# Kernel optimization log

Hardware: AMD Instinct MI355X
Metric: run time of the kernel (lower is better)

The kernel has to match this reference:

```python
import jax, jax.numpy as jnp
import numpy as np

B, S, E, H = 4, 2048, 1024, 16
D = E // H  # head_dim = 64

def setup_inputs() -> dict:
    key = jax.random.key(0)
    k1, k2, k3, k4, k5 = jax.random.split(key, 5)
    x = jax.random.normal(k1, (B, S, E), dtype=jnp.float32)
    # causal mask, broadcast over batch and heads; mask==0 -> -inf
    mask = jnp.tril(jnp.ones((S, S), dtype=jnp.int32))[None, None, :, :]
    Wqkv = jax.random.normal(k2, (E, 3 * E), dtype=jnp.float32) * (1.0 / np.sqrt(E))
    bqkv = jax.random.normal(k3, (3 * E,), dtype=jnp.float32) * 0.02
    Wo = jax.random.normal(k4, (E, E), dtype=jnp.float32) * (1.0 / np.sqrt(E))
    bo = jax.random.normal(k5, (E,), dtype=jnp.float32) * 0.02
    return {"x": x, "mask": mask, "Wqkv": Wqkv, "bqkv": bqkv, "Wo": Wo, "bo": bo}

def reference(x, mask, Wqkv, bqkv, Wo, bo):
    b, s, e = x.shape
    scale = 1.0 / np.sqrt(D)
    qkv = x @ Wqkv + bqkv                      # [b,s,3e]
    qkv = qkv.reshape(b, s, H, 3 * D).transpose(0, 2, 1, 3)  # [b,h,s,3d]
    q, k, v = jnp.split(qkv, 3, axis=-1)       # each [b,h,s,d]
    scores = jnp.einsum('bnqd,bnkd->bnqk', q, k) * scale
    scores = jnp.where(mask == 0, -jnp.inf, scores)
    probs = jax.nn.softmax(scores, axis=-1)
    attn = jnp.einsum('bnqk,bnkd->bnqd', probs, v)  # [b,h,s,d]
    # Faithful to source: reshape (b,h,s,d) -> (b,s,e) WITHOUT transposing back
    attn = attn.reshape(b, s, e)
    return attn @ Wo + bo
```

## Files before the change

### kernel.cpp

```cpp
#include <hip/hip_runtime.h>

typedef __attribute__((ext_vector_type(8))) short bf16x8;
typedef __attribute__((ext_vector_type(4))) float f32x4;
typedef __attribute__((ext_vector_type(2))) unsigned int u32x2;
typedef __attribute__((ext_vector_type(4))) unsigned int u32x4;

#define MFMA16(a, b, c) __builtin_amdgcn_mfma_f32_16x16x32_bf16((a), (b), (c), 0, 0, 0)

#define S_LEN 2048
#define NHEAD 16
#define DHEAD 64
#define BH    64
#define MROWS 8192

__device__ __forceinline__ unsigned short f2bf(float f) {
  unsigned int u = __builtin_bit_cast(unsigned int, f);
  u += 0x7FFFu + ((u >> 16) & 1u);
  return (unsigned short)(u >> 16);
}

__device__ __forceinline__ void gl_lds16(const void* g, void* l) {
  __builtin_amdgcn_global_load_lds(
      (const __attribute__((address_space(1))) void*)g,
      (__attribute__((address_space(3))) void*)l, 16, 0, 0);
}

__device__ __forceinline__ unsigned int pkbf(float lo, float hi) {
  unsigned int ulo = __builtin_bit_cast(unsigned int, lo) + 0x8000u;
  unsigned int uhi = __builtin_bit_cast(unsigned int, hi) + 0x8000u;
  return __builtin_amdgcn_perm(uhi, ulo, 0x07060302u);
}

__global__ __launch_bounds__(256) void cast_bf16(const float* __restrict__ src,
                                                 unsigned short* __restrict__ dst, int n) {
  int i = (blockIdx.x * 256 + threadIdx.x) * 4;
  if (i + 3 < n) {
    f32x4 v = *(const f32x4*)(src + i);
    unsigned long long pk =
        (unsigned long long)f2bf(v[0]) |
        ((unsigned long long)f2bf(v[1]) << 16) |
        ((unsigned long long)f2bf(v[2]) << 32) |
        ((unsigned long long)f2bf(v[3]) << 48);
    *(unsigned long long*)(dst + i) = pk;
  }
}

__global__ __launch_bounds__(256) void transpose_cast(const float* __restrict__ src,
                                                      unsigned short* __restrict__ dst,
                                                      int R, int C) {
  __shared__ float tile[32][33];
  int c0 = blockIdx.x * 32, r0 = blockIdx.y * 32;
  int tx = threadIdx.x, ty = threadIdx.y;
  for (int i = 0; i < 32; i += 8)
    tile[ty + i][tx] = src[(size_t)(r0 + ty + i) * C + c0 + tx];
  __syncthreads();
  for (int i = 0; i < 32; i += 8)
    dst[(size_t)(c0 + ty + i) * R + r0 + tx] = f2bf(tile[tx][ty + i]);
}

__global__ __launch_bounds__(256) void transpose_cast_qkv(const float* __restrict__ src,
                                                          unsigned short* __restrict__ dst) {
  __shared__ float tile[32][33];
  int c0 = blockIdx.x * 32, r0 = blockIdx.y * 32;
  int tx = threadIdx.x, ty = threadIdx.y;
  for (int i = 0; i < 32; i += 8)
    tile[ty + i][tx] = src[(size_t)(r0 + ty + i) * 3072 + c0 + tx];
  __syncthreads();
  for (int i = 0; i < 32; i += 8) {
    int oc = c0 + ty + i;
    int h = oc / 192, rr = oc % 192;
    int nc = ((rr >> 6) << 10) + (h << 6) + (rr & 63);
    dst[(size_t)nc * 1024 + r0 + tx] = f2bf(tile[tx][ty + i]);
  }
}

#define GEMM_CORE(A_, Bt_)                                                              \
  __shared__ unsigned short As[128 * 32];                                               \
  __shared__ unsigned short Bs[128 * 32];                                               \
  const int tid = threadIdx.x;                                                          \
  const int w = tid >> 6, lane = tid & 63, l15 = lane & 15, quad = lane >> 4;           \
  const int wm = w >> 1, wn = w & 1;                                                    \
  const int col0 = blockIdx.x * 128, row0 = blockIdx.y * 128;                           \
  f32x4 acc[4][4] = {};                                                                 \
  for (int kt = 0; kt < 32; ++kt) {                                                     \
    const int k0 = kt * 32;                                                             \
    for (int p = 0; p < 2; ++p) {                                                       \
      int c = p * 256 + tid;                                                            \
      int m = c >> 2, k8 = (c & 3) * 8;                                                 \
      void* ldsA = (char*)As + (size_t)(p * 256 + (tid & 192)) * 16;                    \
      void* ldsB = (char*)Bs + (size_t)(p * 256 + (tid & 192)) * 16;                    \
      gl_lds16(A_ + (size_t)(row0 + m) * 1024 + k0 + k8, ldsA);                         \
      gl_lds16(Bt_ + (size_t)(col0 + m) * 1024 + k0 + k8, ldsB);                        \
    }                                                                                   \
    __syncthreads();                                                                    \
    bf16x8 af[4], bfr[4];                                                               \
    for (int i = 0; i < 4; ++i)                                                         \
      af[i] = *(const bf16x8*)&As[(wm * 64 + i * 16 + l15) * 32 + quad * 8];            \
    for (int j = 0; j < 4; ++j)                                                         \
      bfr[j] = *(const bf16x8*)&Bs[(wn * 64 + j * 16 + l15) * 32 + quad * 8];           \
    for (int i = 0; i < 4; ++i)                                                         \
      for (int j = 0; j < 4; ++j)                                                       \
        acc[i][j] = MFMA16(af[i], bfr[j], acc[i][j]);                                   \
    __syncthreads();                                                                    \
  }


#define VM3 asm volatile("s_waitcnt vmcnt(3)" ::: "memory")
#define VM0 asm volatile("s_waitcnt vmcnt(0)" ::: "memory")
#define BAR __builtin_amdgcn_s_barrier()
#define SB  __builtin_amdgcn_sched_barrier(0)
#define SGB_G(m, n) __builtin_amdgcn_sched_group_barrier((m), (n), 0)

#define SGBPAT                                                                   \
  SGB_G(0x70, 3);                                                                \
  SGB_G(0x8, 2); SGB_G(0x100, 1); SGB_G(0x8, 2); SGB_G(0x100, 1);                \
  SGB_G(0x8, 2); SGB_G(0x100, 1); SGB_G(0x8, 2); SGB_G(0x100, 1);                \
  SGB_G(0x8, 2); SGB_G(0x100, 1); SGB_G(0x8, 2); SGB_G(0x100, 1);                \
  SGB_G(0x8, 2); SGB_G(0x100, 1); SGB_G(0x8, 2); SGB_G(0x100, 1)

#define STAGE3(T, KH, BUF)                                                       \
  do {                                                                           \
    const unsigned short* ga_ = a_src + (T) * 64 + (KH) * 32;                    \
    const unsigned short* gb_ = b_src + (T) * 64 + (KH) * 32;                    \
    char* la_ = SHB + (BUF) * 49152 + (KH) * 8192 + stgo;                        \
    char* lb_ = SHB + (BUF) * 49152 + 16384 + (KH) * 16384 + stgo;               \
    gl_lds16(ga_, la_);                                                          \
    gl_lds16(gb_, lb_);                                                          \
    gl_lds16(gb_ + 131072, lb_ + 8192);                                          \
  } while (0)

#define RDSET(S, BUF, KH)                                                        \
  do {                                                                           \
    const char* Ab_ = SHB + (BUF) * 49152 + (KH) * 8192 + abase;                 \
    const char* Bb_ = SHB + (BUF) * 49152 + 16384 + (KH) * 16384 + bbase;        \
    af##S##0 = *(const bf16x8*)(Ab_);                                            \
    af##S##1 = *(const bf16x8*)(Ab_ + 1024);                                     \
    af##S##2 = *(const bf16x8*)(Ab_ + 2048);                                     \
    af##S##3 = *(const bf16x8*)(Ab_ + 3072);                                     \
    bq##S##0 = *(const bf16x8*)(Bb_);                                            \
    bq##S##1 = *(const bf16x8*)(Bb_ + 1024);                                     \
    bq##S##2 = *(const bf16x8*)(Bb_ + 2048);                                     \
    bq##S##3 = *(const bf16x8*)(Bb_ + 3072);                                     \
  } while (0)

#define MFMA16S(S)                                                               \
  acc[0][0] = MFMA16(af##S##0, bq##S##0, acc[0][0]);                             \
  acc[0][1] = MFMA16(af##S##0, bq##S##1, acc[0][1]);                             \
  acc[0][2] = MFMA16(af##S##0, bq##S##2, acc[0][2]);                             \
  acc[0][3] = MFMA16(af##S##0, bq##S##3, acc[0][3]);                             \
  acc[1][0] = MFMA16(af##S##1, bq##S##0, acc[1][0]);                             \
  acc[1][1] = MFMA16(af##S##1, bq##S##1, acc[1][1]);                             \
  acc[1][2] = MFMA16(af##S##1, bq##S##2, acc[1][2]);                             \
  acc[1][3] = MFMA16(af##S##1, bq##S##3, acc[1][3]);                             \
  acc[2][0] = MFMA16(af##S##2, bq##S##0, acc[2][0]);                             \
  acc[2][1] = MFMA16(af##S##2, bq##S##1, acc[2][1]);                             \
  acc[2][2] = MFMA16(af##S##2, bq##S##2, acc[2][2]);                             \
  acc[2][3] = MFMA16(af##S##2, bq##S##3, acc[2][3]);                             \
  acc[3][0] = MFMA16(af##S##3, bq##S##0, acc[3][0]);                             \
  acc[3][1] = MFMA16(af##S##3, bq##S##1, acc[3][1]);                             \
  acc[3][2] = MFMA16(af##S##3, bq##S##2, acc[3][2]);                             \
  acc[3][3] = MFMA16(af##S##3, bq##S##3, acc[3][3])

#define WND(SP, STG_, VM_, RD_)                                                  \
  {                                                                              \
    STG_;                                                                        \
    __builtin_amdgcn_s_setprio(1);                                               \
    MFMA16S(SP);                                                                 \
    RD_;                                                                         \
    __builtin_amdgcn_s_setprio(0);                                               \
    SGBPAT;                                                                      \
    VM_; SB; BAR; SB;                                                            \
  }

__global__ __launch_bounds__(512, 2) void gemm_qkv(const unsigned short* __restrict__ A,
                                                   const unsigned short* __restrict__ Bt,
                                                   const float* __restrict__ bias,
                                                   unsigned short* __restrict__ Qb,
                                                   unsigned short* __restrict__ Kb,
                                                   unsigned short* __restrict__ Vtb) {
  __shared__ unsigned short SH[49152];
  char* SHB = (char*)SH;
  const int tid = threadIdx.x;
  const int w = tid >> 6, lane = tid & 63, l15 = lane & 15, quad = lane >> 4;
  const int wm = w >> 2, wn = w & 3;
  const int g = ((blockIdx.x & 7) * 96) + (blockIdx.x >> 3);
  const int bx = g % 12, by = g / 12;
  const int col0 = bx << 8, row0 = by << 7;

  const int qa = quad ^ ((l15 >> 1) & 3);
  const int abase = (wm * 64 + l15) * 64 + qa * 16;
  const int bbase = (wn * 64 + l15) * 64 + qa * 16;

  const int qsw = (tid & 3) ^ ((tid >> 3) & 3);
  const unsigned short* a_src = A + (size_t)(row0 + (tid >> 2)) * 1024 + qsw * 8;
  const unsigned short* b_src = Bt + (size_t)(col0 + (tid >> 2)) * 1024 + qsw * 8;
  const int stgo = (tid & ~63) * 16;

  f32x4 acc[4][4] = {};
  bf16x8 afA0, afA1, afA2, afA3, bqA0, bqA1, bqA2, bqA3;
  bf16x8 afB0, afB1, afB2, afB3, bqB0, bqB1, bqB2, bqB3;

  STAGE3(0, 0, 0); STAGE3(0, 1, 0); STAGE3(1, 0, 1);
  VM3; SB; BAR; SB;
  RDSET(A, 0, 0);

  #pragma unroll 1
  for (int jj = 0; jj < 7; ++jj) {
    const int J0 = 2 * jj;
    WND(A, STAGE3(J0 + 1, 1, 1), VM3, RDSET(B, 0, 1))
    WND(B, STAGE3(J0 + 2, 0, 0), VM3, RDSET(A, 1, 0))
    WND(A, STAGE3(J0 + 2, 1, 0), VM3, RDSET(B, 1, 1))
    WND(B, STAGE3(J0 + 3, 0, 1), VM3, RDSET(A, 0, 0))
  }
  WND(A, STAGE3(15, 1, 1), VM3, RDSET(B, 0, 1))
  WND(B, (void)0, VM0, RDSET(A, 1, 0))
  WND(A, (void)0, (void)0, RDSET(B, 1, 1))
  __builtin_amdgcn_s_setprio(1);
  MFMA16S(B);
  __builtin_amdgcn_s_setprio(0);
  __syncthreads();

  const int which = col0 >> 10;
  const int h = ((col0 + wn * 64) >> 6) & 15;
  const int b = row0 >> 11;
  const int srow0 = (row0 & 2047) + wm * 64;
  float bv[4];
  #pragma unroll
  for (int j = 0; j < 4; ++j) {
    int nc = col0 + wn * 64 + j * 16 + l15;
    int oc = ((nc >> 6) & 15) * 192 + (nc >> 10) * 64 + (nc & 63);
    bv[j] = bias[oc];
  }
  float* Ew = (float*)SHB + w * 1072;

  if (which < 2) {
    const float sc = (which == 0) ? 0.18033688011112042f : 1.0f;
    const int lr = lane >> 2, d0 = (lane & 3) * 16;
    unsigned short* base = (which == 0 ? Qb : Kb) + ((size_t)(b * 16 + h) * 2048 + srow0) * 64;
    #pragma unroll
    for (int i = 0; i < 4; ++i) {
      #pragma unroll
      for (int j = 0; j < 4; ++j)
        #pragma unroll
        for (int r = 0; r < 4; ++r)
          Ew[(quad * 4 + r) * 66 + j * 16 + l15] = (acc[i][j][r] + bv[j]) * sc;
      float v[16];
      #pragma unroll
      for (int c = 0; c < 4; ++c)
        *(f32x4*)&v[4 * c] = *(const f32x4*)&Ew[lr * 66 + d0 + 4 * c];
      u32x4 pk0 = {pkbf(v[0], v[1]), pkbf(v[2], v[3]), pkbf(v[4], v[5]), pkbf(v[6], v[7])};
      u32x4 pk1 = {pkbf(v[8], v[9]), pkbf(v[10], v[11]), pkbf(v[12], v[13]), pkbf(v[14], v[15])};
      unsigned short* dst = base + (size_t)(i * 16 + lr) * 64 + d0;
      *(u32x4*)dst = pk0;
      *(u32x4*)(dst + 8) = pk1;
    }
  } else {
    const int d = lane;
    unsigned short* base = Vtb + ((size_t)(b * 16 + h) * 64 + d) * 2048 + srow0;
    #pragma unroll
    for (int i = 0; i < 4; ++i) {
      #pragma unroll
      for (int j = 0; j < 4; ++j)
        #pragma unroll
        for (int r = 0; r < 4; ++r)
          Ew[(quad * 4 + r) * 66 + j * 16 + l15] = acc[i][j][r] + bv[j];
      float e[16];
      #pragma unroll
      for (int k = 0; k < 16; ++k) e[k] = Ew[k * 66 + d];
      u32x4 pk0 = {pkbf(e[0], e[1]), pkbf(e[2], e[3]), pkbf(e[4], e[5]), pkbf(e[6], e[7])};
      u32x4 pk1 = {pkbf(e[8], e[9]), pkbf(e[10], e[11]), pkbf(e[12], e[13]), pkbf(e[14], e[15])};
      unsigned short* dst = base + i * 16;
      *(u32x4*)dst = pk0;
      *(u32x4*)(dst + 8) = pk1;
    }
  }
}

__global__ __launch_bounds__(256) void gemm_out(const unsigned short* __restrict__ A,
                                                const unsigned short* __restrict__ Bt,
                                                const float* __restrict__ bias,
                                                float* __restrict__ out) {
  GEMM_CORE(A, Bt)
  for (int i = 0; i < 4; ++i) {
    int grow = row0 + wm * 64 + i * 16 + quad * 4;
    for (int j = 0; j < 4; ++j) {
      int gcol = col0 + wn * 64 + j * 16 + l15;
      float bvv = bias[gcol];
      for (int r = 0; r < 4; ++r)
        out[(size_t)(grow + r) * 1024 + gcol] = acc[i][j][r] + bvv;
    }
  }
}

__global__ __launch_bounds__(256) void attn_kernel(const unsigned short* __restrict__ Qb,
                                                   const unsigned short* __restrict__ Kb,
                                                   const unsigned short* __restrict__ Vtb,
                                                   unsigned short* __restrict__ attnout) {
  __shared__ unsigned short K0[64 * 32], K1[64 * 32];
  __shared__ unsigned short V0[64 * 32], V1[64 * 32];
  __shared__ unsigned short P0[4][4][512], P1[4][4][512];
  __shared__ float Lbc[4][64];

  const int tid = threadIdx.x;
  const int w = tid >> 6, lane = tid & 63, l15 = lane & 15, quad = lane >> 4;
  const int i2 = blockIdx.x >> 6;
  const int jj = ((i2 & 1) << 1) | ((i2 >> 1) & 1);
  const int qt = (i2 & 4) ? jj : 7 - jj;
  const int bh = blockIdx.x & 63;
  const int q0w = qt * 256 + w * 64;

  const unsigned short* Qg = Qb + (size_t)bh * S_LEN * DHEAD;
  const unsigned short* Kg = Kb + (size_t)bh * S_LEN * DHEAD;
  const unsigned short* Vg = Vtb + (size_t)bh * DHEAD * S_LEN;

  bf16x8 qf[4][2];
  #pragma unroll
  for (int sub = 0; sub < 4; ++sub) {
    const unsigned short* p = Qg + (size_t)(q0w + sub * 16 + l15) * DHEAD + quad * 8;
    qf[sub][0] = *(const bf16x8*)p;
    qf[sub][1] = *(const bf16x8*)(p + 32);
  }

  const int srow = tid >> 2, sc8 = (tid & 3) * 8;
  const unsigned short* kgb = Kg + srow * 64 + sc8;
  const unsigned short* vgb = Vg + (size_t)srow * S_LEN + sc8;
  const int wKo = srow * 32 + sc8;

  const int psw = (l15 & 3) ^ ((l15 >> 2) & 3);
  const int pw0 = l15 * 32 + (((quad >> 1) ^ psw) << 3) + ((quad & 1) << 2);
  const int pw1 = l15 * 32 + ((((quad >> 1) + 2) ^ psw) << 3) + ((quad & 1) << 2);
  const int pro = l15 * 32 + ((quad ^ psw) << 3);
  const int kvo = l15 * 32 + quad * 8;

  f32x4 oacc[4][4] = {};
  float lacc[4] = {0.f, 0.f, 0.f, 0.f};

  const int ktdiag = 4 * qt;
  const int nkt = ktdiag + 4;

  bf16x8 kr0 = *(const bf16x8*)kgb, kr1 = *(const bf16x8*)(kgb + 32);
  bf16x8 vr0 = *(const bf16x8*)vgb, vr1 = *(const bf16x8*)(vgb + 32);

  for (int kt = 0; kt < nkt; ++kt) {
    *(bf16x8*)&K0[wKo] = kr0;  *(bf16x8*)&K1[wKo] = kr1;
    *(bf16x8*)&V0[wKo] = vr0;  *(bf16x8*)&V1[wKo] = vr1;
    __syncthreads();
    if (kt + 1 < nkt) {
      const unsigned short* kp = kgb + (kt + 1) * 4096;
      const unsigned short* vp = vgb + (kt + 1) * 64;
      kr0 = *(const bf16x8*)kp;  kr1 = *(const bf16x8*)(kp + 32);
      vr0 = *(const bf16x8*)vp;  vr1 = *(const bf16x8*)(vp + 32);
    }

    const int t = kt - ktdiag;
    const bool act = (t < 0) || (w >= t);

    if (act) {
      if (t < 0) {
        #pragma unroll
        for (int jk = 0; jk < 4; ++jk) {
          bf16x8 kf0 = *(const bf16x8*)&K0[jk * 512 + kvo];
          bf16x8 kf1 = *(const bf16x8*)&K1[jk * 512 + kvo];
          #pragma unroll
          for (int sub = 0; sub < 4; ++sub) {
            f32x4 z = {};
            z = MFMA16(kf0, qf[sub][0], z);
            z = MFMA16(kf1, qf[sub][1], z);
            float e0 = __builtin_amdgcn_exp2f(z[0]);
            float e1 = __builtin_amdgcn_exp2f(z[1]);
            float e2 = __builtin_amdgcn_exp2f(z[2]);
            float e3 = __builtin_amdgcn_exp2f(z[3]);
            lacc[sub] += (e0 + e1) + (e2 + e3);
            unsigned short* pd = (jk < 2) ? P0[w][sub] : P1[w][sub];
            *(u32x2*)&pd[(jk & 1) ? pw1 : pw0] = (u32x2){pkbf(e0, e1), pkbf(e2, e3)};
          }
        }
      } else {
        const bool dg = (t == w);
        #pragma unroll
        for (int jk = 0; jk < 4; ++jk) {
          bf16x8 kf0 = *(const bf16x8*)&K0[jk * 512 + kvo];
          bf16x8 kf1 = *(const bf16x8*)&K1[jk * 512 + kvo];
          #pragma unroll
          for (int sub = 0; sub < 4; ++sub) {
            unsigned short* pd = (jk < 2) ? P0[w][sub] : P1[w][sub];
            unsigned int* dst = (unsigned int*)&pd[(jk & 1) ? pw1 : pw0];
            if (dg && jk > sub) { *(u32x2*)dst = (u32x2){0u, 0u}; continue; }
            f32x4 z = {};
            z = MFMA16(kf0, qf[sub][0], z);
            z = MFMA16(kf1, qf[sub][1], z);
            if (dg && jk == sub) {
              #pragma unroll
              for (int r = 0; r < 4; ++r)
                if (quad * 4 + r > l15) z[r] = -3e38f;
            }
            float e0 = __builtin_amdgcn_exp2f(z[0]);
            float e1 = __builtin_amdgcn_exp2f(z[1]);
            float e2 = __builtin_amdgcn_exp2f(z[2]);
            float e3 = __builtin_amdgcn_exp2f(z[3]);
            lacc[sub] += (e0 + e1) + (e2 + e3);
            *(u32x2*)dst = (u32x2){pkbf(e0, e1), pkbf(e2, e3)};
          }
        }
      }

      bf16x8 pf[4][2];
      #pragma unroll
      for (int sub = 0; sub < 4; ++sub) {
        pf[sub][0] = *(const bf16x8*)&P0[w][sub][pro];
        pf[sub][1] = *(const bf16x8*)&P1[w][sub][pro];
      }
      #pragma unroll
      for (int dt = 0; dt < 4; ++dt) {
        bf16x8 vb0 = *(const bf16x8*)&V0[dt * 512 + kvo];
        bf16x8 vb1 = *(const bf16x8*)&V1[dt * 512 + kvo];
        #pragma unroll
        for (int sub = 0; sub < 4; ++sub) {
          oacc[sub][dt] = MFMA16(pf[sub][0], vb0, oacc[sub][dt]);
          oacc[sub][dt] = MFMA16(pf[sub][1], vb1, oacc[sub][dt]);
        }
      }
    }
    __syncthreads();
  }

  #pragma unroll
  for (int sub = 0; sub < 4; ++sub) {
    float l = lacc[sub];
    l += __shfl_xor(l, 16);
    l += __shfl_xor(l, 32);
    if (quad == 0) Lbc[w][sub * 16 + l15] = l;
  }
  #pragma unroll
  for (int sub = 0; sub < 4; ++sub) {
    f32x4 l4 = *(const f32x4*)&Lbc[w][sub * 16 + quad * 4];
    int qbase = q0w + sub * 16 + quad * 4;
    unsigned short* dst = attnout + ((size_t)bh * S_LEN + qbase) * DHEAD;
    #pragma unroll
    for (int r = 0; r < 4; ++r) {
      float inv = __builtin_amdgcn_rcpf(l4[r]);
      #pragma unroll
      for (int dt = 0; dt < 4; ++dt)
        dst[(size_t)r * DHEAD + dt * 16 + l15] = f2bf(oacc[sub][dt][r] * inv);
    }
  }
}

extern "C" void kernel_launch(void* const* d_in, const int* in_sizes, int n_in,
                              void* d_out, int out_size, void* d_ws, size_t ws_size,
                              hipStream_t stream) {
  const float* x    = (const float*)d_in[0];
  const float* Wqkv = (const float*)d_in[2];
  const float* bqkv = (const float*)d_in[3];
  const float* Wo   = (const float*)d_in[4];
  const float* bo   = (const float*)d_in[5];
  float* out = (float*)d_out;

  char* ws = (char*)d_ws;
  unsigned short* Xbf   = (unsigned short*)(ws);
  unsigned short* WqkvT = (unsigned short*)(ws + 16777216);
  unsigned short* WoT   = (unsigned short*)(ws + 23068672);
  unsigned short* Qb    = (unsigned short*)(ws + 25165824);
  unsigned short* Kb    = (unsigned short*)(ws + 41943040);
  unsigned short* Vtb   = (unsigned short*)(ws + 58720256);
  unsigned short* Attn  = (unsigned short*)(ws + 75497472);

  cast_bf16<<<8192, 256, 0, stream>>>(x, Xbf, MROWS * 1024);
  transpose_cast_qkv<<<dim3(96, 32), dim3(32, 8), 0, stream>>>(Wqkv, WqkvT);
  transpose_cast<<<dim3(32, 32), dim3(32, 8), 0, stream>>>(Wo, WoT, 1024, 1024);
  gemm_qkv<<<768, 512, 0, stream>>>(Xbf, WqkvT, bqkv, Qb, Kb, Vtb);
  attn_kernel<<<512, 256, 0, stream>>>(Qb, Kb, Vtb, Attn);
  gemm_out<<<dim3(8, 64), 256, 0, stream>>>(Attn, WoT, bo, out);
}
```

Before: 275.2 us.

## Reuse pipelined 128x256 QKV GEMM main loop for output projection GEMM

```diff
diff --git a/kernel.cpp b/kernel.cpp
--- a/kernel.cpp
+++ b/kernel.cpp
@@ -73,36 +73,6 @@
     dst[(size_t)nc * 1024 + r0 + tx] = f2bf(tile[tx][ty + i]);
   }
 }
-
-#define GEMM_CORE(A_, Bt_)                                                              \
-  __shared__ unsigned short As[128 * 32];                                               \
-  __shared__ unsigned short Bs[128 * 32];                                               \
-  const int tid = threadIdx.x;                                                          \
-  const int w = tid >> 6, lane = tid & 63, l15 = lane & 15, quad = lane >> 4;           \
-  const int wm = w >> 1, wn = w & 1;                                                    \
-  const int col0 = blockIdx.x * 128, row0 = blockIdx.y * 128;                           \
-  f32x4 acc[4][4] = {};                                                                 \
-  for (int kt = 0; kt < 32; ++kt) {                                                     \
-    const int k0 = kt * 32;                                                             \
-    for (int p = 0; p < 2; ++p) {                                                       \
-      int c = p * 256 + tid;                                                            \
-      int m = c >> 2, k8 = (c & 3) * 8;                                                 \
-      void* ldsA = (char*)As + (size_t)(p * 256 + (tid & 192)) * 16;                    \
-      void* ldsB = (char*)Bs + (size_t)(p * 256 + (tid & 192)) * 16;                    \
-      gl_lds16(A_ + (size_t)(row0 + m) * 1024 + k0 + k8, ldsA);                         \
-      gl_lds16(Bt_ + (size_t)(col0 + m) * 1024 + k0 + k8, ldsB);                        \
-    }                                                                                   \
-    __syncthreads();                                                                    \
-    bf16x8 af[4], bfr[4];                                                               \
-    for (int i = 0; i < 4; ++i)                                                         \
-      af[i] = *(const bf16x8*)&As[(wm * 64 + i * 16 + l15) * 32 + quad * 8];            \
-    for (int j = 0; j < 4; ++j)                                                         \
-      bfr[j] = *(const bf16x8*)&Bs[(wn * 64 + j * 16 + l15) * 32 + quad * 8];           \
-    for (int i = 0; i < 4; ++i)                                                         \
-      for (int j = 0; j < 4; ++j)                                                       \
-        acc[i][j] = MFMA16(af[i], bfr[j], acc[i][j]);                                   \
-    __syncthreads();                                                                    \
-  }
 
 
 #define VM3 asm volatile("s_waitcnt vmcnt(3)" ::: "memory")
@@ -172,6 +142,26 @@
     VM_; SB; BAR; SB;                                                            \
   }
 
+#define GEMM256_KLOOP                                                            \
+  STAGE3(0, 0, 0); STAGE3(0, 1, 0); STAGE3(1, 0, 1);                             \
+  VM3; SB; BAR; SB;                                                              \
+  RDSET(A, 0, 0);                                                                \
+  _Pragma("unroll 1")                                                            \
+  for (int jj = 0; jj < 7; ++jj) {                                               \
+    const int J0 = 2 * jj;                                                       \
+    WND(A, STAGE3(J0 + 1, 1, 1), VM3, RDSET(B, 0, 1))                            \
+    WND(B, STAGE3(J0 + 2, 0, 0), VM3, RDSET(A, 1, 0))                            \
+    WND(A, STAGE3(J0 + 2, 1, 0), VM3, RDSET(B, 1, 1))                            \
+    WND(B, STAGE3(J0 + 3, 0, 1), VM3, RDSET(A, 0, 0))                            \
+  }                                                                              \
+  WND(A, STAGE3(15, 1, 1), VM3, RDSET(B, 0, 1))                                  \
+  WND(B, (void)0, VM0, RDSET(A, 1, 0))                                           \
+  WND(A, (void)0, (void)0, RDSET(B, 1, 1))                                       \
+  __builtin_amdgcn_s_setprio(1);                                                 \
+  MFMA16S(B);                                                                    \
+  __builtin_amdgcn_s_setprio(0);                                                 \
+  __syncthreads();
+
 __global__ __launch_bounds__(512, 2) void gemm_qkv(const unsigned short* __restrict__ A,
                                                    const unsigned short* __restrict__ Bt,
                                                    const float* __restrict__ bias,
@@ -200,25 +190,7 @@
   bf16x8 afA0, afA1, afA2, afA3, bqA0, bqA1, bqA2, bqA3;
   bf16x8 afB0, afB1, afB2, afB3, bqB0, bqB1, bqB2, bqB3;
 
-  STAGE3(0, 0, 0); STAGE3(0, 1, 0); STAGE3(1, 0, 1);
-  VM3; SB; BAR; SB;
-  RDSET(A, 0, 0);
-
-  #pragma unroll 1
-  for (int jj = 0; jj < 7; ++jj) {
-    const int J0 = 2 * jj;
-    WND(A, STAGE3(J0 + 1, 1, 1), VM3, RDSET(B, 0, 1))
-    WND(B, STAGE3(J0 + 2, 0, 0), VM3, RDSET(A, 1, 0))
-    WND(A, STAGE3(J0 + 2, 1, 0), VM3, RDSET(B, 1, 1))
-    WND(B, STAGE3(J0 + 3, 0, 1), VM3, RDSET(A, 0, 0))
-  }
-  WND(A, STAGE3(15, 1, 1), VM3, RDSET(B, 0, 1))
-  WND(B, (void)0, VM0, RDSET(A, 1, 0))
-  WND(A, (void)0, (void)0, RDSET(B, 1, 1))
-  __builtin_amdgcn_s_setprio(1);
-  MFMA16S(B);
-  __builtin_amdgcn_s_setprio(0);
-  __syncthreads();
+  GEMM256_KLOOP
 
   const int which = col0 >> 10;
   const int h = ((col0 + wn * 64) >> 6) & 15;
@@ -276,18 +248,45 @@
   }
 }
 
-__global__ __launch_bounds__(256) void gemm_out(const unsigned short* __restrict__ A,
-                                                const unsigned short* __restrict__ Bt,
-                                                const float* __restrict__ bias,
-                                                float* __restrict__ out) {
-  GEMM_CORE(A, Bt)
+__global__ __launch_bounds__(512, 2) void gemm_out(const unsigned short* __restrict__ A,
+                                                   const unsigned short* __restrict__ Bt,
+                                                   const float* __restrict__ bias,
+                                                   float* __restrict__ out) {
+  __shared__ unsigned short SH[49152];
+  char* SHB = (char*)SH;
+  const int tid = threadIdx.x;
+  const int w = tid >> 6, lane = tid & 63, l15 = lane & 15, quad = lane >> 4;
+  const int wm = w >> 2, wn = w & 3;
+  const int g = ((blockIdx.x & 7) * 32) + (blockIdx.x >> 3);
+  const int bx = g & 3, by = g >> 2;
+  const int col0 = bx << 8, row0 = by << 7;
+
+  const int qa = quad ^ ((l15 >> 1) & 3);
+  const int abase = (wm * 64 + l15) * 64 + qa * 16;
+  const int bbase = (wn * 64 + l15) * 64 + qa * 16;
+
+  const int qsw = (tid & 3) ^ ((tid >> 3) & 3);
+  const unsigned short* a_src = A + (size_t)(row0 + (tid >> 2)) * 1024 + qsw * 8;
+  const unsigned short* b_src = Bt + (size_t)(col0 + (tid >> 2)) * 1024 + qsw * 8;
+  const int stgo = (tid & ~63) * 16;
+
+  f32x4 acc[4][4] = {};
+  bf16x8 afA0, afA1, afA2, afA3, bqA0, bqA1, bqA2, bqA3;
+  bf16x8 afB0, afB1, afB2, afB3, bqB0, bqB1, bqB2, bqB3;
+
+  GEMM256_KLOOP
+
+  const int grow0 = row0 + wm * 64;
+  const int gcol0 = col0 + wn * 64;
+  #pragma unroll
   for (int i = 0; i < 4; ++i) {
-    int grow = row0 + wm * 64 + i * 16 + quad * 4;
+    #pragma unroll
     for (int j = 0; j < 4; ++j) {
-      int gcol = col0 + wn * 64 + j * 16 + l15;
-      float bvv = bias[gcol];
+      const int gcol = gcol0 + j * 16 + l15;
+      const float bvv = bias[gcol];
+      #pragma unroll
       for (int r = 0; r < 4; ++r)
-        out[(size_t)(grow + r) * 1024 + gcol] = acc[i][j][r] + bvv;
+        out[(size_t)(grow0 + i * 16 + quad * 4 + r) * 1024 + gcol] = acc[i][j][r] + bvv;
     }
   }
 }
@@ -470,5 +469,5 @@
   transpose_cast<<<dim3(32, 32), dim3(32, 8), 0, stream>>>(Wo, WoT, 1024, 1024);
   gemm_qkv<<<768, 512, 0, stream>>>(Xbf, WqkvT, bqkv, Qb, Kb, Vtb);
   attn_kernel<<<512, 256, 0, stream>>>(Qb, Kb, Vtb, Attn);
-  gemm_out<<<dim3(8, 64), 256, 0, stream>>>(Attn, WoT, bo, out);
-}
+  gemm_out<<<256, 512, 0, stream>>>(Attn, WoT, bo, out);
+}
```

Result: no change. 270.8 us (-1.6%).
